# Kernel tuning notes

Hardware: AMD Instinct MI355X
Metric: run time of the kernel (lower is better)

## Reference

```python
import jax, jax.numpy as jnp
import numpy as np

N, H, E, ATTR = 50000, 256, 800000, 107


def _ln(x, g, b, eps=1e-5):
    mu = jnp.mean(x, axis=-1, keepdims=True)
    v = jnp.mean((x - mu) ** 2, axis=-1, keepdims=True)
    return (x - mu) * jax.lax.rsqrt(v + eps) * g + b


def _gcn(x, src, dst, ew, W, b, n):
    # PyG GCNConv with edge_weight: add self-loops (weight 1), symmetric norm
    loop = jnp.arange(n)
    src = jnp.concatenate([src, loop])
    dst = jnp.concatenate([dst, loop])
    ew = jnp.concatenate([ew, jnp.ones((n,), ew.dtype)])
    deg = jax.ops.segment_sum(ew, dst, num_segments=n)  # [n]
    dinv = jnp.where(deg > 0, jax.lax.rsqrt(deg), 0.0)
    norm = dinv[src] * ew * dinv[dst]  # [E+n]
    h = x @ W.T  # [n,H] linear transform first
    agg = jax.ops.segment_sum(norm[:, None] * h[src], dst, num_segments=n)
    return agg + b


def setup_inputs() -> dict:
    key = jax.random.key(0)
    ks = jax.random.split(key, 12)
    s = 1.0 / np.sqrt(H)
    return {
        "x_struct": jax.random.normal(ks[0], (N, H), jnp.float32),
        "edge_index_bold": jax.random.randint(ks[1], (2, E), 0, N),
        "edge_attr_bold": jax.random.uniform(ks[2], (E,), jnp.float32),  # positive weights
        "edge_index_temp": jax.random.randint(ks[3], (2, E), 0, N),
        "edge_attr_temp": jax.random.uniform(ks[4], (E, ATTR), jnp.float32),
        "Wb": jax.random.normal(ks[5], (H, H), jnp.float32) * s,
        "bb": jnp.zeros((H,), jnp.float32),
        "Wt": jax.random.normal(ks[6], (H, H), jnp.float32) * s,
        "bt": jnp.zeros((H,), jnp.float32),
        "W1": jax.random.normal(ks[7], (H, ATTR), jnp.float32) * (1.0 / np.sqrt(ATTR)),
        "b1": jnp.zeros((H,), jnp.float32),
        "g1": jnp.ones((H,), jnp.float32),
        "be1": jnp.zeros((H,), jnp.float32),
        "W2": jax.random.normal(ks[8], (1, H), jnp.float32) * 0.01,
        "b2": jnp.ones((1,), jnp.float32),  # keep temporal edge weights positive
        "gs": jnp.ones((H,), jnp.float32),
        "bs": jnp.zeros((H,), jnp.float32),
        "gt": jnp.ones((H,), jnp.float32),
        "btn": jnp.zeros((H,), jnp.float32),
    }


def reference(x_struct, edge_attr_bold, edge_attr_temp, Wb, bb, Wt, bt,
              W1, b1, g1, be1, W2, b2, gs, bs, gt, btn,
              edge_index_bold, edge_index_temp):
    x = x_struct
    orig = x
    # BOLD-correlation GCN stage: gcn -> residual -> LN -> ReLU
    out = _gcn(x, edge_index_bold[0], edge_index_bold[1], edge_attr_bold, Wb, bb, N)
    x = jax.nn.relu(_ln(out + x, gs, bs))
    # temporal edge-weight MLP: Linear(107->H) -> LN -> ReLU -> Linear(H->1) -> squeeze
    h = jax.nn.relu(_ln(edge_attr_temp @ W1.T + b1, g1, be1))
    w = (h @ W2.T + b2)[:, 0]  # [E]
    # temporal GCN stage: gcn -> residual -> LN -> ReLU
    out = _gcn(x, edge_index_temp[0], edge_index_temp[1], w, Wt, bt, N)
    x = jax.nn.relu(_ln(out + x, gt, btn))
    # final residual with original input through struct_norm
    return _ln(x + orig, gs, bs)
```

## Files before the change

kernel.cpp:

```cpp
#include <hip/hip_runtime.h>

#define HDIM 256
#define KA 107
#define KAP 128

typedef short bf16x8 __attribute__((ext_vector_type(8)));
typedef float f32x4 __attribute__((ext_vector_type(4)));
typedef unsigned short ushort_t;

__device__ inline unsigned short f2bf(float f) {
    union { float f; unsigned u; } v; v.f = f;
    unsigned r = v.u + 0x7fff + ((v.u >> 16) & 1);
    return (unsigned short)(r >> 16);
}

__device__ inline unsigned cvt_pk_bf16(float a, float b) {
    unsigned r;
    asm("v_cvt_pk_bf16_f32 %0, %1, %2" : "=v"(r) : "v"(a), "v"(b));
    return r;
}

__device__ inline float bf_lo(unsigned u) { union { unsigned v; float f; } x; x.v = u << 16; return x.f; }
__device__ inline float bf_hi(unsigned u) { union { unsigned v; float f; } x; x.v = u & 0xffff0000u; return x.f; }

__device__ inline float4 guarded_load4(const float* p, size_t off, size_t tot) {
    if (off + 4 <= tot) return *(const float4*)(p + off);
    float4 r = {0.f, 0.f, 0.f, 0.f};
    float* rr = (float*)&r;
    for (int e = 0; e < 4; ++e) if (off + e < tot) rr[e] = p[off + e];
    return r;
}


__global__ void hist_cnt_kernel(const int* __restrict__ dst, int* cnt, int ne) {
    int e = blockIdx.x * 256 + threadIdx.x;
    if (e < ne) atomicAdd(&cnt[dst[e]], 1);
}

__global__ void f32_to_bf16_kernel(const float* __restrict__ in, ushort_t* __restrict__ out, int n4) {
    int i = blockIdx.x * 256 + threadIdx.x;
    if (i < n4) {
        float4 v = ((const float4*)in)[i];
        uint2 o;
        o.x = cvt_pk_bf16(v.x, v.y);
        o.y = cvt_pk_bf16(v.z, v.w);
        ((uint2*)out)[i] = o;
    }
}

__global__ __launch_bounds__(256) void scan_a_kernel(const int* __restrict__ cnt,
                                                     int* __restrict__ bsum, int n) {
    const int tid = threadIdx.x;
    const int i = blockIdx.x * 256 + tid;
    int v = (i < n) ? cnt[i] : 0;
    int s = v;
#pragma unroll
    for (int d = 1; d < 64; d <<= 1) s += __shfl_xor(s, d);
    __shared__ int ws[4];
    if ((tid & 63) == 0) ws[tid >> 6] = s;
    __syncthreads();
    if (tid == 0) bsum[blockIdx.x] = ws[0] + ws[1] + ws[2] + ws[3];
}

__global__ __launch_bounds__(256) void scan_b_kernel(int* __restrict__ bsum, int nb) {
    const int tid = threadIdx.x;
    int v = (tid < nb) ? bsum[tid] : 0;
    const int lane = tid & 63, wid = tid >> 6;
    int incl = v;
#pragma unroll
    for (int d = 1; d < 64; d <<= 1) { int m = __shfl_up(incl, d); if (lane >= d) incl += m; }
    __shared__ int ws[4];
    if (lane == 63) ws[wid] = incl;
    __syncthreads();
    if (tid < 4) {
        int wv = ws[tid];
        int iv = wv;
#pragma unroll
        for (int d = 1; d < 4; d <<= 1) { int m = __shfl_up(iv, d, 4); if (tid >= d) iv += m; }
        ws[tid] = iv - wv;
    }
    __syncthreads();
    if (tid < nb) bsum[tid] = (incl - v) + ws[wid];
}

__global__ __launch_bounds__(256) void scan_c_kernel(const int* __restrict__ cnt,
                                                     const int* __restrict__ bsum,
                                                     int* __restrict__ rptr,
                                                     int* __restrict__ cur, int n) {
    const int tid = threadIdx.x;
    const int i = blockIdx.x * 256 + tid;
    int v = (i < n) ? cnt[i] : 0;
    const int lane = tid & 63, wid = tid >> 6;
    int incl = v;
#pragma unroll
    for (int d = 1; d < 64; d <<= 1) { int m = __shfl_up(incl, d); if (lane >= d) incl += m; }
    __shared__ int ws[4];
    if (lane == 63) ws[wid] = incl;
    __syncthreads();
    if (tid < 4) {
        int wv = ws[tid];
        int iv = wv;
#pragma unroll
        for (int d = 1; d < 4; d <<= 1) { int m = __shfl_up(iv, d, 4); if (tid >= d) iv += m; }
        ws[tid] = iv - wv;
    }
    __syncthreads();
    const int excl = (incl - v) + ws[wid] + bsum[blockIdx.x];
    if (i < n) { rptr[i] = excl; cur[i] = excl; }
    if (i == n - 1) rptr[n] = excl + v;
}

__global__ void fill_kernel(const int* __restrict__ src, const int* __restrict__ dst,
                            const float* __restrict__ w,
                            int* cur, uint2* __restrict__ edata, int ne) {
    int e = blockIdx.x * 256 + threadIdx.x;
    if (e < ne) {
        int d = dst[e];
        int pos = atomicAdd(&cur[d], 1);
        uint2 ed;
        ed.x = (unsigned)src[e];
        ed.y = __float_as_uint(w[e]);
        edata[pos] = ed;
    }
}

__global__ void deg_kernel(const uint2* __restrict__ edata, const int* __restrict__ rptr,
                           float* __restrict__ dinv, int n) {
    int v = blockIdx.x * 256 + threadIdx.x;
    if (v < n) {
        const int b = rptr[v], e = rptr[v + 1];
        float s = 1.0f;
        for (int i = b; i < e; ++i) s += __uint_as_float(edata[i].y);
        dinv[v] = s > 0.f ? rsqrtf(s) : 0.f;
    }
}

__global__ __launch_bounds__(256) void agg_kernel(const ushort_t* __restrict__ Xb,
                                                  const int* __restrict__ rptr,
                                                  const uint2* __restrict__ edata,
                                                  const float* __restrict__ dinv,
                                                  ushort_t* __restrict__ out, int n) {
    const int v = blockIdx.x * 4 + (threadIdx.x >> 6);
    if (v >= n) return;
    const int lane = threadIdx.x & 63;
    const float dv = dinv[v];
    const uint2 xv = *(const uint2*)(Xb + (size_t)v * HDIM + lane * 4);
    const float dv2 = dv * dv;
    float a0[8], a1[8], a2[8], a3[8];
#pragma unroll
    for (int c = 0; c < 8; ++c) { a0[c] = 0.f; a1[c] = 0.f; a2[c] = 0.f; a3[c] = 0.f; }
    a0[0] = dv2 * bf_lo(xv.x); a1[0] = dv2 * bf_hi(xv.x);
    a2[0] = dv2 * bf_lo(xv.y); a3[0] = dv2 * bf_hi(xv.y);

    const int b = rptr[v];
    const int total = rptr[v + 1] - b;
    uint2 pv[8]; float pn[8];
#pragma unroll
    for (int c = 0; c < 8; ++c) {
        if (c < total) {
            uint2 ed = edata[b + c];
            pn[c] = dinv[ed.x] * __uint_as_float(ed.y) * dv;
            pv[c] = *(const uint2*)(Xb + (size_t)ed.x * HDIM + lane * 4);
        }
    }
    for (int base = 0; base < total; base += 8) {
#pragma unroll
        for (int c = 0; c < 8; ++c) {
            if (base + c < total) {
                uint2 cv = pv[c]; float cn = pn[c];
                int nx = base + 8 + c;
                if (nx < total) {
                    uint2 ed = edata[b + nx];
                    pn[c] = dinv[ed.x] * __uint_as_float(ed.y) * dv;
                    pv[c] = *(const uint2*)(Xb + (size_t)ed.x * HDIM + lane * 4);
                }
                a0[c] = fmaf(cn, bf_lo(cv.x), a0[c]);
                a1[c] = fmaf(cn, bf_hi(cv.x), a1[c]);
                a2[c] = fmaf(cn, bf_lo(cv.y), a2[c]);
                a3[c] = fmaf(cn, bf_hi(cv.y), a3[c]);
            }
        }
    }
    float r0 = ((a0[0] + a0[1]) + (a0[2] + a0[3])) + ((a0[4] + a0[5]) + (a0[6] + a0[7]));
    float r1 = ((a1[0] + a1[1]) + (a1[2] + a1[3])) + ((a1[4] + a1[5]) + (a1[6] + a1[7]));
    float r2 = ((a2[0] + a2[1]) + (a2[2] + a2[3])) + ((a2[4] + a2[5]) + (a2[6] + a2[7]));
    float r3 = ((a3[0] + a3[1]) + (a3[2] + a3[3])) + ((a3[4] + a3[5]) + (a3[6] + a3[7]));
    uint2 o;
    o.x = cvt_pk_bf16(r0, r1);
    o.y = cvt_pk_bf16(r2, r3);
    *(uint2*)(out + (size_t)v * HDIM + lane * 4) = o;
}

__global__ void prep_w_kernel(const float* __restrict__ W, ushort_t* __restrict__ Wp,
                              int K, int KP) {
    int i = blockIdx.x * 256 + threadIdx.x;
    if (i < 256 * KP) {
        int n = i / KP, k = i - n * KP;
        Wp[i] = (k < K) ? f2bf(W[n * K + k]) : (ushort_t)0;
    }
}

__global__ __launch_bounds__(256) void mlp_mfma_kernel(
    const float* __restrict__ A,
    const ushort_t* __restrict__ Wp,
    const float* __restrict__ b1v, const float* __restrict__ g1v,
    const float* __restrict__ be1v, const float* __restrict__ W2,
    const float* __restrict__ b2s, float* __restrict__ out,
    int M, int ntiles) {
    __shared__ ushort_t As[2][64][136];
    __shared__ float ps1[64][4], ps2[64][4], pd[64][4];
    const int tid = threadIdx.x;
    const int l = tid & 63, wv = tid >> 6, g = l >> 4, c = l & 15;
    const float b2sc = b2s[0];
    const size_t tot = (size_t)M * KA;

    for (int z = tid; z < 2 * 64 * 16; z += 256) {
        int buf = z >> 10;
        int rem = z & 1023;
        As[buf][rem >> 4][112 + (rem & 15)] = 0;
    }

    bf16x8 wreg[4][4];
    {
        const ushort_t* wb = Wp + (size_t)(wv * 64 + c) * KAP + g * 8;
#pragma unroll
        for (int ks = 0; ks < 4; ++ks)
#pragma unroll
            for (int nt = 0; nt < 4; ++nt)
                wreg[ks][nt] = *(const bf16x8*)(wb + nt * 16 * KAP + ks * 32);
    }

    const int srow = tid >> 2, sj = tid & 3;
    float4 sreg[7];

    const int t0 = blockIdx.x;
    if (t0 < ntiles) {
        const size_t roff = (size_t)(t0 * 64 + srow) * KA + sj * 4;
#pragma unroll
        for (int i = 0; i < 7; ++i) sreg[i] = guarded_load4(A, roff + i * 16, tot);
#pragma unroll
        for (int i = 0; i < 7; ++i) {
            uint2 o;
            o.x = cvt_pk_bf16(sreg[i].x, sreg[i].y);
            o.y = cvt_pk_bf16(sreg[i].z, sreg[i].w);
            *(uint2*)&As[0][srow][sj * 4 + i * 16] = o;
        }
    }
    __syncthreads();

    int cur = 0;
    for (int t = t0; t < ntiles; t += gridDim.x) {
        const int tn = t + gridDim.x;
        const bool have_next = tn < ntiles;
        if (have_next) {
            const size_t roff = (size_t)(tn * 64 + srow) * KA + sj * 4;
#pragma unroll
            for (int i = 0; i < 7; ++i) sreg[i] = guarded_load4(A, roff + i * 16, tot);
        }

        f32x4 acc[4][4];
#pragma unroll
        for (int rt = 0; rt < 4; ++rt)
#pragma unroll
            for (int nt = 0; nt < 4; ++nt) acc[rt][nt] = (f32x4){0.f, 0.f, 0.f, 0.f};
        __builtin_amdgcn_s_setprio(1);
#pragma unroll
        for (int ks = 0; ks < 4; ++ks) {
            bf16x8 af[4];
#pragma unroll
            for (int rt = 0; rt < 4; ++rt)
                af[rt] = *(const bf16x8*)&As[cur][rt * 16 + c][ks * 32 + g * 8];
#pragma unroll
            for (int nt = 0; nt < 4; ++nt)
#pragma unroll
                for (int rt = 0; rt < 4; ++rt)
                    acc[rt][nt] = __builtin_amdgcn_mfma_f32_16x16x32_bf16(wreg[ks][nt], af[rt], acc[rt][nt], 0, 0, 0);
        }
        __builtin_amdgcn_s_setprio(0);

        const int nb = wv * 64 + (g << 2);
        const int m0 = t * 64;
#pragma unroll
        for (int rt = 0; rt < 4; ++rt) {
            float s1 = 0.f, s2 = 0.f;
#pragma unroll
            for (int nt = 0; nt < 4; ++nt) {
                const float4 b4 = *(const float4*)(b1v + nb + nt * 16);
                f32x4 v = acc[rt][nt];
                v[0] += b4.x; v[1] += b4.y; v[2] += b4.z; v[3] += b4.w;
                acc[rt][nt] = v;
                s1 += v[0] + v[1] + v[2] + v[3];
                s2 += v[0] * v[0] + v[1] * v[1] + v[2] * v[2] + v[3] * v[3];
            }
            s1 += __shfl_xor(s1, 16); s1 += __shfl_xor(s1, 32);
            s2 += __shfl_xor(s2, 16); s2 += __shfl_xor(s2, 32);
            if (l < 16) { ps1[rt * 16 + c][wv] = s1; ps2[rt * 16 + c][wv] = s2; }
        }
        __syncthreads();
#pragma unroll
        for (int rt = 0; rt < 4; ++rt) {
            float4 p1 = *(const float4*)ps1[rt * 16 + c];
            float4 p2 = *(const float4*)ps2[rt * 16 + c];
            float s1 = p1.x + p1.y + p1.z + p1.w;
            float s2 = p2.x + p2.y + p2.z + p2.w;
            float mu = s1 * (1.f / HDIM);
            float var = s2 * (1.f / HDIM) - mu * mu;
            float rs = rsqrtf(var + 1e-5f);
            float dacc = 0.f;
#pragma unroll
            for (int nt = 0; nt < 4; ++nt) {
                const float4 g4 = *(const float4*)(g1v + nb + nt * 16);
                const float4 e4 = *(const float4*)(be1v + nb + nt * 16);
                const float4 w4 = *(const float4*)(W2 + nb + nt * 16);
                f32x4 v = acc[rt][nt];
                float y0 = fmaxf((v[0] - mu) * rs * g4.x + e4.x, 0.f);
                float y1 = fmaxf((v[1] - mu) * rs * g4.y + e4.y, 0.f);
                float y2 = fmaxf((v[2] - mu) * rs * g4.z + e4.z, 0.f);
                float y3 = fmaxf((v[3] - mu) * rs * g4.w + e4.w, 0.f);
                dacc = fmaf(y0, w4.x, dacc); dacc = fmaf(y1, w4.y, dacc);
                dacc = fmaf(y2, w4.z, dacc); dacc = fmaf(y3, w4.w, dacc);
            }
            dacc += __shfl_xor(dacc, 16); dacc += __shfl_xor(dacc, 32);
            if (l < 16) pd[rt * 16 + c][wv] = dacc;
        }
        if (have_next) {
#pragma unroll
            for (int i = 0; i < 7; ++i) {
                uint2 o;
                o.x = cvt_pk_bf16(sreg[i].x, sreg[i].y);
                o.y = cvt_pk_bf16(sreg[i].z, sreg[i].w);
                *(uint2*)&As[cur ^ 1][srow][sj * 4 + i * 16] = o;
            }
        }
        __syncthreads();
        if (tid < 64) {
            float4 p = *(const float4*)pd[tid];
            int gr = m0 + tid;
            if (gr < M) out[gr] = p.x + p.y + p.z + p.w + b2sc;
        }
        cur ^= 1;
    }
}

template <int MODE>
__global__ __launch_bounds__(256) void gemm_node_kernel(
    const ushort_t* __restrict__ A,
    const ushort_t* __restrict__ Wp,
    const float* __restrict__ bias,
    const ushort_t* __restrict__ res_bf,
    const ushort_t* __restrict__ orig_bf,
    const float* __restrict__ g1v, const float* __restrict__ b1v,
    const float* __restrict__ g2v, const float* __restrict__ b2v,
    float* __restrict__ out, ushort_t* __restrict__ out_bf, int M) {
    __shared__ ushort_t As[64][264];
    __shared__ float ps1[64][4], ps2[64][4], ps3[64][4], ps4[64][4];
    const int tid = threadIdx.x;
    const int m0 = blockIdx.x * 64;
    const int l = tid & 63, wv = tid >> 6, g = l >> 4, c = l & 15;

    {
        const int r = tid >> 2, j = tid & 3;
        const ushort_t* gsrc = A + (size_t)(m0 + r) * HDIM;
        const bool ok = (m0 + r) < M;
#pragma unroll
        for (int i = 0; i < 8; ++i) {
            const int ci = i * 4 + j;
            bf16x8 v = (bf16x8){0,0,0,0,0,0,0,0};
            if (ok) v = *(const bf16x8*)(gsrc + ci * 8);
            *(bf16x8*)&As[r][ci * 8] = v;
        }
    }
    __syncthreads();

    f32x4 acc[4][4];
#pragma unroll
    for (int rt = 0; rt < 4; ++rt)
#pragma unroll
        for (int nt = 0; nt < 4; ++nt) acc[rt][nt] = (f32x4){0.f, 0.f, 0.f, 0.f};

    const ushort_t* wb = Wp + (size_t)(wv * 64 + c) * HDIM + g * 8;
    __builtin_amdgcn_s_setprio(1);
#pragma unroll
    for (int ks = 0; ks < 8; ++ks) {
        bf16x8 af[4];
#pragma unroll
        for (int rt = 0; rt < 4; ++rt)
            af[rt] = *(const bf16x8*)&As[rt * 16 + c][ks * 32 + g * 8];
#pragma unroll
        for (int nt = 0; nt < 4; ++nt) {
            bf16x8 bfr = *(const bf16x8*)(wb + nt * 16 * HDIM + ks * 32);
#pragma unroll
            for (int rt = 0; rt < 4; ++rt)
                acc[rt][nt] = __builtin_amdgcn_mfma_f32_16x16x32_bf16(bfr, af[rt], acc[rt][nt], 0, 0, 0);
        }
    }
    __builtin_amdgcn_s_setprio(0);

    const int nb = wv * 64 + (g << 2);
#pragma unroll
    for (int rt = 0; rt < 4; ++rt) {
        const int m = m0 + rt * 16 + c;
        const bool vm = m < M;
        const ushort_t* rrow = res_bf + (size_t)m * HDIM + nb;
        float s1 = 0.f, s2 = 0.f;
#pragma unroll
        for (int nt = 0; nt < 4; ++nt) {
            const float4 b4 = *(const float4*)(bias + nb + nt * 16);
            float4 r4 = {0.f, 0.f, 0.f, 0.f};
            if (vm) {
                uint2 rb = *(const uint2*)(rrow + nt * 16);
                r4.x = bf_lo(rb.x); r4.y = bf_hi(rb.x);
                r4.z = bf_lo(rb.y); r4.w = bf_hi(rb.y);
            }
            f32x4 v = acc[rt][nt];
            v[0] += b4.x + r4.x; v[1] += b4.y + r4.y;
            v[2] += b4.z + r4.z; v[3] += b4.w + r4.w;
            acc[rt][nt] = v;
            s1 += v[0] + v[1] + v[2] + v[3];
            s2 += v[0] * v[0] + v[1] * v[1] + v[2] * v[2] + v[3] * v[3];
        }
        s1 += __shfl_xor(s1, 16); s1 += __shfl_xor(s1, 32);
        s2 += __shfl_xor(s2, 16); s2 += __shfl_xor(s2, 32);
        if (l < 16) { ps1[rt * 16 + c][wv] = s1; ps2[rt * 16 + c][wv] = s2; }
    }
    __syncthreads();
#pragma unroll
    for (int rt = 0; rt < 4; ++rt) {
        const int m = m0 + rt * 16 + c;
        const bool vm = m < M;
        float4 p1 = *(const float4*)ps1[rt * 16 + c];
        float4 p2 = *(const float4*)ps2[rt * 16 + c];
        float s1 = p1.x + p1.y + p1.z + p1.w;
        float s2 = p2.x + p2.y + p2.z + p2.w;
        float mu = s1 * (1.f / HDIM);
        float var = s2 * (1.f / HDIM) - mu * mu;
        float rs = rsqrtf(var + 1e-5f);
        if constexpr (MODE == 0) {
            ushort_t* obrow = out_bf + (size_t)m * HDIM + nb;
#pragma unroll
            for (int nt = 0; nt < 4; ++nt) {
                const float4 g4 = *(const float4*)(g1v + nb + nt * 16);
                const float4 e4 = *(const float4*)(b1v + nb + nt * 16);
                f32x4 v = acc[rt][nt];
                float o0 = fmaxf((v[0] - mu) * rs * g4.x + e4.x, 0.f);
                float o1 = fmaxf((v[1] - mu) * rs * g4.y + e4.y, 0.f);
                float o2 = fmaxf((v[2] - mu) * rs * g4.z + e4.z, 0.f);
                float o3 = fmaxf((v[3] - mu) * rs * g4.w + e4.w, 0.f);
                if (vm) {
                    uint2 ob;
                    ob.x = cvt_pk_bf16(o0, o1);
                    ob.y = cvt_pk_bf16(o2, o3);
                    *(uint2*)(obrow + nt * 16) = ob;
                }
            }
        } else {
            const ushort_t* grow = orig_bf + (size_t)m * HDIM + nb;
            float t1 = 0.f, t2 = 0.f;
#pragma unroll
            for (int nt = 0; nt < 4; ++nt) {
                const float4 g4 = *(const float4*)(g1v + nb + nt * 16);
                const float4 e4 = *(const float4*)(b1v + nb + nt * 16);
                float4 o4 = {0.f, 0.f, 0.f, 0.f};
                if (vm) {
                    uint2 gb = *(const uint2*)(grow + nt * 16);
                    o4.x = bf_lo(gb.x); o4.y = bf_hi(gb.x);
                    o4.z = bf_lo(gb.y); o4.w = bf_hi(gb.y);
                }
                f32x4 v = acc[rt][nt];
                f32x4 u;
                u[0] = fmaxf((v[0] - mu) * rs * g4.x + e4.x, 0.f) + o4.x;
                u[1] = fmaxf((v[1] - mu) * rs * g4.y + e4.y, 0.f) + o4.y;
                u[2] = fmaxf((v[2] - mu) * rs * g4.z + e4.z, 0.f) + o4.z;
                u[3] = fmaxf((v[3] - mu) * rs * g4.w + e4.w, 0.f) + o4.w;
                acc[rt][nt] = u;
                t1 += u[0] + u[1] + u[2] + u[3];
                t2 += u[0] * u[0] + u[1] * u[1] + u[2] * u[2] + u[3] * u[3];
            }
            t1 += __shfl_xor(t1, 16); t1 += __shfl_xor(t1, 32);
            t2 += __shfl_xor(t2, 16); t2 += __shfl_xor(t2, 32);
            if (l < 16) { ps3[rt * 16 + c][wv] = t1; ps4[rt * 16 + c][wv] = t2; }
        }
    }
    if constexpr (MODE == 1) {
        __syncthreads();
#pragma unroll
        for (int rt = 0; rt < 4; ++rt) {
            const int m = m0 + rt * 16 + c;
            const bool vm = m < M;
            float4 p1 = *(const float4*)ps3[rt * 16 + c];
            float4 p2 = *(const float4*)ps4[rt * 16 + c];
            float s1 = p1.x + p1.y + p1.z + p1.w;
            float s2 = p2.x + p2.y + p2.z + p2.w;
            float mu2 = s1 * (1.f / HDIM);
            float var2 = s2 * (1.f / HDIM) - mu2 * mu2;
            float rs2 = rsqrtf(var2 + 1e-5f);
            float* orow = out + (size_t)m * HDIM + nb;
#pragma unroll
            for (int nt = 0; nt < 4; ++nt) {
                const float4 g4 = *(const float4*)(g2v + nb + nt * 16);
                const float4 e4 = *(const float4*)(b2v + nb + nt * 16);
                f32x4 u = acc[rt][nt];
                float4 o;
                o.x = (u[0] - mu2) * rs2 * g4.x + e4.x;
                o.y = (u[1] - mu2) * rs2 * g4.y + e4.y;
                o.z = (u[2] - mu2) * rs2 * g4.z + e4.z;
                o.w = (u[3] - mu2) * rs2 * g4.w + e4.w;
                if (vm) *(float4*)(orow + nt * 16) = o;
            }
        }
    }
}


extern "C" void kernel_launch(void* const* d_in, const int* in_sizes, int n_in,
                              void* d_out, int out_size, void* d_ws, size_t ws_size,
                              hipStream_t stream) {
    const float* x    = (const float*)d_in[0];
    const int*   eib  = (const int*)d_in[1];
    const float* eab  = (const float*)d_in[2];
    const int*   eit  = (const int*)d_in[3];
    const float* eat  = (const float*)d_in[4];
    const float* Wb   = (const float*)d_in[5];
    const float* bb   = (const float*)d_in[6];
    const float* Wt   = (const float*)d_in[7];
    const float* bt   = (const float*)d_in[8];
    const float* W1   = (const float*)d_in[9];
    const float* b1   = (const float*)d_in[10];
    const float* g1   = (const float*)d_in[11];
    const float* be1  = (const float*)d_in[12];
    const float* W2   = (const float*)d_in[13];
    const float* b2   = (const float*)d_in[14];
    const float* gs   = (const float*)d_in[15];
    const float* bs   = (const float*)d_in[16];
    const float* gt   = (const float*)d_in[17];
    const float* btn  = (const float*)d_in[18];

    const int Nn = in_sizes[0] / HDIM;
    const int Ne = in_sizes[2];

    const int* src_b = eib;  const int* dst_b = eib + Ne;
    const int* src_t = eit;  const int* dst_t = eit + Ne;

    char* w = (char*)d_ws;
    ushort_t* aggb = (ushort_t*)w; w += (size_t)Nn * HDIM * 2;
    ushort_t* xb   = (ushort_t*)w; w += (size_t)Nn * HDIM * 2;
    ushort_t* x1b  = (ushort_t*)w; w += (size_t)Nn * HDIM * 2;
    float*    wtmp = (float*)w;    w += (size_t)Ne * 4;
    float*    dinv = (float*)w;    w += (size_t)Nn * 4;
    int*      cnt  = (int*)w;      w += (size_t)Nn * 4;
    int*      rptr = (int*)w;      w += (size_t)(Nn + 4) * 4;
    int*      cur  = (int*)w;      w += (size_t)Nn * 4;
    uint2*    edata = (uint2*)w;   w += (size_t)Ne * 8;
    int*      bsum = (int*)w;      w += (size_t)256 * 4;
    ushort_t* W1p  = (ushort_t*)w; w += (size_t)256 * KAP * 2;
    ushort_t* Wbp  = (ushort_t*)w; w += (size_t)256 * 256 * 2;
    ushort_t* Wtp  = (ushort_t*)w; w += (size_t)256 * 256 * 2;

    float* out = (float*)d_out;
    dim3 b256(256);
    dim3 gN((Nn + 255) / 256), gE((Ne + 255) / 256);
    const int nbScan = (Nn + 255) / 256;
    dim3 gAgg((Nn + 3) / 4);
    dim3 gGemmN((Nn + 63) / 64);
    const int ntiles = (Ne + 63) / 64;
    dim3 gMlp(512);
    const int n4 = Nn * HDIM / 4;
    dim3 gCvt((n4 + 255) / 256);

    prep_w_kernel<<<dim3((256 * KAP + 255) / 256), b256, 0, stream>>>(W1, W1p, KA, KAP);
    prep_w_kernel<<<dim3((256 * 256 + 255) / 256), b256, 0, stream>>>(Wb, Wbp, 256, 256);
    prep_w_kernel<<<dim3((256 * 256 + 255) / 256), b256, 0, stream>>>(Wt, Wtp, 256, 256);
    f32_to_bf16_kernel<<<gCvt, b256, 0, stream>>>(x, xb, n4);

    hipMemsetAsync(cnt, 0, (size_t)Nn * 4, stream);
    hist_cnt_kernel<<<gE, b256, 0, stream>>>(dst_b, cnt, Ne);
    scan_a_kernel<<<dim3(nbScan), b256, 0, stream>>>(cnt, bsum, Nn);
    scan_b_kernel<<<dim3(1), b256, 0, stream>>>(bsum, nbScan);
    scan_c_kernel<<<dim3(nbScan), b256, 0, stream>>>(cnt, bsum, rptr, cur, Nn);
    fill_kernel<<<gE, b256, 0, stream>>>(src_b, dst_b, eab, cur, edata, Ne);
    deg_kernel<<<gN, b256, 0, stream>>>(edata, rptr, dinv, Nn);
    agg_kernel<<<gAgg, b256, 0, stream>>>(xb, rptr, edata, dinv, aggb, Nn);
    gemm_node_kernel<0><<<gGemmN, b256, 0, stream>>>(
        aggb, Wbp, bb, xb, nullptr, gs, bs, nullptr, nullptr, nullptr, x1b, Nn);

    mlp_mfma_kernel<<<gMlp, b256, 0, stream>>>(
        eat, W1p, b1, g1, be1, W2, b2, wtmp, Ne, ntiles);

    hipMemsetAsync(cnt, 0, (size_t)Nn * 4, stream);
    hist_cnt_kernel<<<gE, b256, 0, stream>>>(dst_t, cnt, Ne);
    scan_a_kernel<<<dim3(nbScan), b256, 0, stream>>>(cnt, bsum, Nn);
    scan_b_kernel<<<dim3(1), b256, 0, stream>>>(bsum, nbScan);
    scan_c_kernel<<<dim3(nbScan), b256, 0, stream>>>(cnt, bsum, rptr, cur, Nn);
    fill_kernel<<<gE, b256, 0, stream>>>(src_t, dst_t, wtmp, cur, edata, Ne);
    deg_kernel<<<gN, b256, 0, stream>>>(edata, rptr, dinv, Nn);
    agg_kernel<<<gAgg, b256, 0, stream>>>(x1b, rptr, edata, dinv, aggb, Nn);
    gemm_node_kernel<1><<<gGemmN, b256, 0, stream>>>(
        aggb, Wtp, bt, x1b, xb, gt, btn, gs, bs, out, nullptr, Nn);
}
```

Baseline: 776.0 us.

## Give each wave full rows in edge MLP to drop cross-wave LayerNorm reduction

New measurement: 1.571 ms. +102.5%, slower.

```diff
diff --git a/kernel.cpp b/kernel.cpp
--- a/kernel.cpp
+++ b/kernel.cpp
@@ -208,7 +208,6 @@
     const float* __restrict__ b2s, float* __restrict__ out,
     int M, int ntiles) {
     __shared__ ushort_t As[2][64][136];
-    __shared__ float ps1[64][4], ps2[64][4], pd[64][4];
     const int tid = threadIdx.x;
     const int l = tid & 63, wv = tid >> 6, g = l >> 4, c = l & 15;
     const float b2sc = b2s[0];
@@ -218,16 +217,6 @@
         int buf = z >> 10;
         int rem = z & 1023;
         As[buf][rem >> 4][112 + (rem & 15)] = 0;
-    }
-
-    bf16x8 wreg[4][4];
-    {
-        const ushort_t* wb = Wp + (size_t)(wv * 64 + c) * KAP + g * 8;
-#pragma unroll
-        for (int ks = 0; ks < 4; ++ks)
-#pragma unroll
-            for (int nt = 0; nt < 4; ++nt)
-                wreg[ks][nt] = *(const bf16x8*)(wb + nt * 16 * KAP + ks * 32);
     }
 
     const int srow = tid >> 2, sj = tid & 3;
@@ -248,6 +237,7 @@
     }
     __syncthreads();
 
+    const int nb = g << 2;
     int cur = 0;
     for (int t = t0; t < ntiles; t += gridDim.x) {
         const int tn = t + gridDim.x;
@@ -258,71 +248,60 @@
             for (int i = 0; i < 7; ++i) sreg[i] = guarded_load4(A, roff + i * 16, tot);
         }
 
-        f32x4 acc[4][4];
-#pragma unroll
-        for (int rt = 0; rt < 4; ++rt)
-#pragma unroll
-            for (int nt = 0; nt < 4; ++nt) acc[rt][nt] = (f32x4){0.f, 0.f, 0.f, 0.f};
+        f32x4 acc[16];
+#pragma unroll
+        for (int nt = 0; nt < 16; ++nt) acc[nt] = (f32x4){0.f, 0.f, 0.f, 0.f};
+        bf16x8 af[4];
+#pragma unroll
+        for (int ks = 0; ks < 4; ++ks)
+            af[ks] = *(const bf16x8*)&As[cur][wv * 16 + c][ks * 32 + g * 8];
         __builtin_amdgcn_s_setprio(1);
 #pragma unroll
-        for (int ks = 0; ks < 4; ++ks) {
-            bf16x8 af[4];
-#pragma unroll
-            for (int rt = 0; rt < 4; ++rt)
-                af[rt] = *(const bf16x8*)&As[cur][rt * 16 + c][ks * 32 + g * 8];
-#pragma unroll
-            for (int nt = 0; nt < 4; ++nt)
-#pragma unroll
-                for (int rt = 0; rt < 4; ++rt)
-                    acc[rt][nt] = __builtin_amdgcn_mfma_f32_16x16x32_bf16(wreg[ks][nt], af[rt], acc[rt][nt], 0, 0, 0);
+        for (int nt = 0; nt < 16; ++nt) {
+            const ushort_t* wb = Wp + (size_t)(nt * 16 + c) * KAP + g * 8;
+#pragma unroll
+            for (int ks = 0; ks < 4; ++ks) {
+                bf16x8 wfr = *(const bf16x8*)(wb + ks * 32);
+                acc[nt] = __builtin_amdgcn_mfma_f32_16x16x32_bf16(wfr, af[ks], acc[nt], 0, 0, 0);
+            }
         }
         __builtin_amdgcn_s_setprio(0);
 
-        const int nb = wv * 64 + (g << 2);
-        const int m0 = t * 64;
-#pragma unroll
-        for (int rt = 0; rt < 4; ++rt) {
-            float s1 = 0.f, s2 = 0.f;
-#pragma unroll
-            for (int nt = 0; nt < 4; ++nt) {
-                const float4 b4 = *(const float4*)(b1v + nb + nt * 16);
-                f32x4 v = acc[rt][nt];
-                v[0] += b4.x; v[1] += b4.y; v[2] += b4.z; v[3] += b4.w;
-                acc[rt][nt] = v;
-                s1 += v[0] + v[1] + v[2] + v[3];
-                s2 += v[0] * v[0] + v[1] * v[1] + v[2] * v[2] + v[3] * v[3];
-            }
-            s1 += __shfl_xor(s1, 16); s1 += __shfl_xor(s1, 32);
-            s2 += __shfl_xor(s2, 16); s2 += __shfl_xor(s2, 32);
-            if (l < 16) { ps1[rt * 16 + c][wv] = s1; ps2[rt * 16 + c][wv] = s2; }
-        }
-        __syncthreads();
-#pragma unroll
-        for (int rt = 0; rt < 4; ++rt) {
-            float4 p1 = *(const float4*)ps1[rt * 16 + c];
-            float4 p2 = *(const float4*)ps2[rt * 16 + c];
-            float s1 = p1.x + p1.y + p1.z + p1.w;
-            float s2 = p2.x + p2.y + p2.z + p2.w;
-            float mu = s1 * (1.f / HDIM);
-            float var = s2 * (1.f / HDIM) - mu * mu;
-            float rs = rsqrtf(var + 1e-5f);
-            float dacc = 0.f;
-#pragma unroll
-            for (int nt = 0; nt < 4; ++nt) {
-                const float4 g4 = *(const float4*)(g1v + nb + nt * 16);
-                const float4 e4 = *(const float4*)(be1v + nb + nt * 16);
-                const float4 w4 = *(const float4*)(W2 + nb + nt * 16);
-                f32x4 v = acc[rt][nt];
-                float y0 = fmaxf((v[0] - mu) * rs * g4.x + e4.x, 0.f);
-                float y1 = fmaxf((v[1] - mu) * rs * g4.y + e4.y, 0.f);
-                float y2 = fmaxf((v[2] - mu) * rs * g4.z + e4.z, 0.f);
-                float y3 = fmaxf((v[3] - mu) * rs * g4.w + e4.w, 0.f);
-                dacc = fmaf(y0, w4.x, dacc); dacc = fmaf(y1, w4.y, dacc);
-                dacc = fmaf(y2, w4.z, dacc); dacc = fmaf(y3, w4.w, dacc);
-            }
-            dacc += __shfl_xor(dacc, 16); dacc += __shfl_xor(dacc, 32);
-            if (l < 16) pd[rt * 16 + c][wv] = dacc;
-        }
+        float s1 = 0.f, s2 = 0.f;
+#pragma unroll
+        for (int nt = 0; nt < 16; ++nt) {
+            const float4 b4 = *(const float4*)(b1v + nt * 16 + nb);
+            f32x4 v = acc[nt];
+            v[0] += b4.x; v[1] += b4.y; v[2] += b4.z; v[3] += b4.w;
+            acc[nt] = v;
+            s1 += v[0] + v[1] + v[2] + v[3];
+            s2 += v[0] * v[0] + v[1] * v[1] + v[2] * v[2] + v[3] * v[3];
+        }
+        s1 += __shfl_xor(s1, 16); s1 += __shfl_xor(s1, 32);
+        s2 += __shfl_xor(s2, 16); s2 += __shfl_xor(s2, 32);
+        const float mu = s1 * (1.f / HDIM);
+        const float var = s2 * (1.f / HDIM) - mu * mu;
+        const float rs = rsqrtf(var + 1e-5f);
+        float dacc = 0.f;
+#pragma unroll
+        for (int nt = 0; nt < 16; ++nt) {
+            const float4 g4 = *(const float4*)(g1v + nt * 16 + nb);
+            const float4 e4 = *(const float4*)(be1v + nt * 16 + nb);
+            const float4 w4 = *(const float4*)(W2 + nt * 16 + nb);
+            f32x4 v = acc[nt];
+            float y0 = fmaxf((v[0] - mu) * rs * g4.x + e4.x, 0.f);
+            float y1 = fmaxf((v[1] - mu) * rs * g4.y + e4.y, 0.f);
+            float y2 = fmaxf((v[2] - mu) * rs * g4.z + e4.z, 0.f);
+            float y3 = fmaxf((v[3] - mu) * rs * g4.w + e4.w, 0.f);
+            dacc = fmaf(y0, w4.x, dacc); dacc = fmaf(y1, w4.y, dacc);
+            dacc = fmaf(y2, w4.z, dacc); dacc = fmaf(y3, w4.w, dacc);
+        }
+        dacc += __shfl_xor(dacc, 16); dacc += __shfl_xor(dacc, 32);
+        if (l < 16) {
+            int gr = t * 64 + wv * 16 + c;
+            if (gr < M) out[gr] = dacc + b2sc;
+        }
+
         if (have_next) {
 #pragma unroll
             for (int i = 0; i < 7; ++i) {
@@ -333,11 +312,6 @@
             }
         }
         __syncthreads();
-        if (tid < 64) {
-            float4 p = *(const float4*)pd[tid];
-            int gr = m0 + tid;
-            if (gr < M) out[gr] = p.x + p.y + p.z + p.w + b2sc;
-        }
         cur ^= 1;
     }
 }
@@ -563,7 +537,7 @@
     dim3 gAgg((Nn + 3) / 4);
     dim3 gGemmN((Nn + 63) / 64);
     const int ntiles = (Ne + 63) / 64;
-    dim3 gMlp(512);
+    dim3 gMlp(1024);
     const int n4 = Nn * HDIM / 4;
     dim3 gCvt((n4 + 255) / 256);
 
```
